# Optimization experiments

Hardware: AMD Instinct MI355X
Metric: run time of the kernel (lower is better)

Reference implementation:

```python
import jax, jax.numpy as jnp
import numpy as np

P = 0.8  # DropConnect keep probability
KERNELS = (3, 2)


def eps_contract(core, x, ks):
    """Contract one EPS core with all sliding ks x ks windows of x.
    core: (out, q**(ks*ks)); x: (b, h, w, q) -> (b, h-ks+1, w-ks+1, out).
    Builds the window tensor-product incrementally (small fixed ks*ks loop)."""
    b, h, w, q = x.shape
    H, W = h - ks + 1, w - ks + 1
    prod = None
    for di in range(ks):
        for dj in range(ks):
            pix = x[:, di:di + H, dj:dj + W, :]  # (b, H, W, q)
            if prod is None:
                prod = pix
            else:
                prod = (prod[..., :, None] * pix[..., None, :]).reshape(b, H, W, -1)
    # prod: (b, H, W, q**(ks*ks))
    return jnp.einsum('bhwk,ok->bhwo', prod, core)


def dropconnect_epses(epses):
    """Bernoulli(P) mask each core's components, rescale by 1/P (training mode)."""
    mkey = jax.random.key(42)
    out = []
    for i, core in enumerate(epses):
        mask = (jax.random.uniform(jax.random.fold_in(mkey, i), core.shape) < P).astype(core.dtype)
        out.append(mask * core / P)
    return out


def setup_inputs() -> dict:
    key = jax.random.key(0)
    k0, k1, k2, k3 = jax.random.split(key, 4)
    b = 128
    x = jax.random.uniform(k0, (b, 28, 28, 2), jnp.float32)  # quantum-encoded image
    d0 = 2 ** (3 * 3)   # 512 : first core input dim (q=2, ks=3)
    d1 = 6 ** (2 * 2)   # 1296: second core input dim (q=6, ks=2)
    eps0 = jax.random.normal(k1, (6, d0), jnp.float32) * d0 ** -0.5
    eps1 = jax.random.normal(k2, (10, d1), jnp.float32) * d1 ** -0.5
    in_features = 25 * 25 * 10  # (28 - (3+2) + 2)^2 * out_q
    W = jax.random.normal(k3, (10, in_features), jnp.float32) * (in_features ** -0.5 / 4.0)
    bias = jnp.zeros((10,), jnp.float32)
    return {"x": x, "eps0": eps0, "eps1": eps1, "W": W, "bias": bias}


def reference(x, eps0, eps1, W, bias):
    e0, e1 = dropconnect_epses((eps0, eps1))
    h = eps_contract(e0, x, KERNELS[0])   # (b, 26, 26, 6)
    h = eps_contract(e1, h, KERNELS[1])   # (b, 25, 25, 10)
    flat = h.reshape(h.shape[0], -1)      # b (h w q)
    return flat @ W.T + bias
```

## Files before the change

### kernel.cpp

```cpp
#include <hip/hip_runtime.h>
#include <hip/hip_bf16.h>
#include <stdint.h>

typedef __attribute__((ext_vector_type(8))) short short8;
typedef __attribute__((ext_vector_type(4))) float floatx4;
typedef __attribute__((ext_vector_type(4))) int intx4;

__device__ float h_g[128 * 4056];
__device__ unsigned short bsw1_g[8192];
__device__ unsigned short bsw2c_g[14400];

__device__ __forceinline__ void threefry2x32(uint32_t k0, uint32_t k1,
                                             uint32_t& x0, uint32_t& x1) {
  const uint32_t ks2 = k0 ^ k1 ^ 0x1BD11BDAu;
  uint32_t ks[3] = {k0, k1, ks2};
  const int rot[8] = {13, 15, 26, 6, 17, 29, 16, 24};
  x0 += ks[0];
  x1 += ks[1];
#pragma unroll
  for (int i = 0; i < 5; ++i) {
#pragma unroll
    for (int j = 0; j < 4; ++j) {
      const int r = rot[(i & 1) * 4 + j];
      x0 += x1;
      x1 = (x1 << r) | (x1 >> (32 - r));
      x1 ^= x0;
    }
    x0 += ks[(i + 1) % 3];
    x1 += ks[(i + 2) % 3] + (uint32_t)(i + 1);
  }
}

struct TFPair { uint32_t x0, x1; };
constexpr TFPair tf_const(uint32_t k0, uint32_t k1, uint32_t x0, uint32_t x1) {
  const uint32_t ks2 = k0 ^ k1 ^ 0x1BD11BDAu;
  uint32_t ks[3] = {k0, k1, ks2};
  const int rot[8] = {13, 15, 26, 6, 17, 29, 16, 24};
  x0 += ks[0];
  x1 += ks[1];
  for (int i = 0; i < 5; ++i) {
    for (int j = 0; j < 4; ++j) {
      const int r = rot[(i & 1) * 4 + j];
      x0 += x1;
      x1 = (x1 << r) | (x1 >> (32 - r));
      x1 ^= x0;
    }
    x0 += ks[(i + 1) % 3];
    x1 += ks[(i + 2) % 3] + (uint32_t)(i + 1);
  }
  return {x0, x1};
}
constexpr TFPair FOLD0 = tf_const(0u, 42u, 0u, 0u);
constexpr TFPair FOLD1 = tf_const(0u, 42u, 0u, 1u);

__device__ __forceinline__ float dropmask(int core, int e, float v) {
  const uint32_t f0 = core ? FOLD1.x0 : FOLD0.x0;
  const uint32_t f1 = core ? FOLD1.x1 : FOLD0.x1;
  uint32_t a = 0u, b = (uint32_t)e;
  threefry2x32(f0, f1, a, b);
  uint32_t bits = a ^ b;
  float u = __uint_as_float((bits >> 9) | 0x3F800000u) - 1.0f;
  float m = (u < 0.8f) ? 1.0f : 0.0f;
  return v * m / 0.8f;
}

__device__ __forceinline__ unsigned short f2bf(float f) {
  uint32_t u = __float_as_uint(f);
  uint32_t r = u + 0x7fffu + ((u >> 16) & 1u);
  return (unsigned short)(r >> 16);
}

union B2I { __hip_bfloat162 b; int i; };
__device__ __forceinline__ int pk_bf16(float lo, float hi) {
  B2I u;
  u.b = __float22bfloat162_rn(make_float2(lo, hi));
  return u.i;
}
union Frag { intx4 i; short8 s; };

__global__ void prep_kernel(const float* __restrict__ eps0,
                            const float* __restrict__ eps1,
                            const float* __restrict__ bias,
                            float* __restrict__ out) {
  int idx = blockIdx.x * 256 + threadIdx.x;
  if (idx < 1280) out[idx] = bias[idx % 10];
  if (idx < 8192) {
    int j = idx & 7, L = (idx >> 3) & 63, c = idx >> 9;
    int o = L & 15, q = L >> 4;
    int k = c * 32 + q * 8 + j;
    float v = 0.0f;
    if (o < 6) {
      int e = o * 512 + k;
      v = dropmask(0, e, eps0[e]);
    }
    bsw1_g[idx] = f2bf(v);
  } else if (idx < 22592) {
    int s = idx - 8192;
    int j = s & 7;
    int wl = (s >> 3) % 40;
    int c = (s >> 3) / 40;
    int o = wl % 10, q = wl / 10;
    int t = 45 * q + c;
    int m = t / 5, nk = 8 * (t % 5) + j;
    float v = 0.0f;
    if (nk < 36) {
      int e = o * 1296 + m * 36 + nk;
      v = dropmask(1, e, eps1[e]);
    }
    bsw2c_g[s] = f2bf(v);
  }
}

__global__ __launch_bounds__(256, 8) void stage1_kernel(
    const float* __restrict__ x) {
  __shared__ intx4 b1s[1024];

  const int b = blockIdx.y;
  const int tid = threadIdx.x;

  {
    const intx4* bsrc1 = (const intx4*)bsw1_g;
#pragma unroll
    for (int i = 0; i < 4; ++i) b1s[i * 256 + tid] = bsrc1[i * 256 + tid];
  }
  __syncthreads();

  const int t1 = blockIdx.x * 4 + (tid >> 6);
  if (t1 >= 43) return;
  const int lane = tid & 63;
  const int col = lane & 15, q = lane >> 4;

  const float2* x2 = (const float2*)x + b * 784;
  const int p_raw = t1 * 16 + col;
  const int p = p_raw < 676 ? p_raw : 675;
  const int ii = p / 26, jj = p - (p / 26) * 26;

  float xv[9][2];
#pragma unroll
  for (int di = 0; di < 3; ++di)
#pragma unroll
    for (int dj = 0; dj < 3; ++dj) {
      float2 v = x2[(ii + di) * 28 + (jj + dj)];
      xv[di * 3 + dj][0] = v.x;
      xv[di * 3 + dj][1] = v.y;
    }

  float w3[8];
#pragma unroll
  for (int j = 0; j < 8; ++j)
    w3[j] = xv[6][(j >> 2) & 1] * xv[7][(j >> 1) & 1] * xv[8][j & 1];

  const float wq = xv[4][(q >> 1) & 1] * xv[5][q & 1];
  float t01[4], t23[4];
#pragma unroll
  for (int a = 0; a < 2; ++a)
#pragma unroll
    for (int d = 0; d < 2; ++d) {
      t01[a * 2 + d] = xv[0][a] * xv[1][d];
      t23[a * 2 + d] = xv[2][a] * xv[3][d] * wq;
    }

  floatx4 acc0 = {0.f, 0.f, 0.f, 0.f};
  floatx4 acc1 = {0.f, 0.f, 0.f, 0.f};
#pragma unroll
  for (int c = 0; c < 16; ++c) {
    Frag bf;
    bf.i = b1s[c * 64 + lane];
    const float w = t01[c >> 2] * t23[c & 3];
    Frag af;
    af.i.x = pk_bf16(w * w3[0], w * w3[1]);
    af.i.y = pk_bf16(w * w3[2], w * w3[3]);
    af.i.z = pk_bf16(w * w3[4], w * w3[5]);
    af.i.w = pk_bf16(w * w3[6], w * w3[7]);
    if (c & 1)
      acc1 = __builtin_amdgcn_mfma_f32_16x16x32_bf16(af.s, bf.s, acc1, 0, 0, 0);
    else
      acc0 = __builtin_amdgcn_mfma_f32_16x16x32_bf16(af.s, bf.s, acc0, 0, 0, 0);
  }
  const floatx4 acc = acc0 + acc1;
  if (col < 6) {
#pragma unroll
    for (int r = 0; r < 4; ++r) {
      const int pp = t1 * 16 + q * 4 + r;
      if (pp < 676) h_g[b * 4056 + pp * 6 + col] = acc[r];
    }
  }
}

__global__ __launch_bounds__(512, 6) void stage2_kernel(
    const float* __restrict__ W, float* __restrict__ out) {
  __shared__ intx4 b2s[1800];
  __shared__ float hs[1092];
  __shared__ float flat_t[8][160];

  const int b = blockIdx.y;
  const int tg = blockIdx.x;
  const int tid = threadIdx.x;
  const int wv = tid >> 6;
  const int lane = tid & 63;
  const int col = lane & 15, q = lane >> 4;
  const int colc = col < 10 ? col : 9;

  {
    const intx4* bsrc2g = (const intx4*)bsw2c_g;
#pragma unroll 1
    for (int i = tid; i < 1800; i += 512) b2s[i] = bsrc2g[i];
  }

  const int r_lo = (tg * 128) / 25;
  const int nrow = (26 - r_lo) < 7 ? (26 - r_lo) : 7;
  const int nflt = nrow * 156;
  for (int i = tid; i < nflt; i += 512) hs[i] = h_g[b * 4056 + r_lo * 156 + i];
  __syncthreads();

  const int tile = tg * 8 + wv;
  const int base2 = tile * 16;
  const int p_raw = base2 + col;
  const int p = p_raw < 625 ? p_raw : 624;
  const int prow = (p * 41) >> 10;
  const int pcol = p - prow * 25;
  const int lr = prow - r_lo;
  const int hbase = (lr * 26 + pcol) * 6;

  float h10r[6], h11r[6];
#pragma unroll
  for (int t = 0; t < 6; ++t) {
    h10r[t] = hs[hbase + 156 + t];
    h11r[t] = hs[hbase + 162 + t];
  }

  floatx4 acc0 = {0.f, 0.f, 0.f, 0.f};
  floatx4 acc1 = {0.f, 0.f, 0.f, 0.f};
#pragma unroll
  for (int d = 0; d < 9; ++d) {
    const int m = 9 * q + d;
    const int ia = (m * 43) >> 8;
    const int ic = m - ia * 6;
    const float p01 = hs[hbase + ia] * hs[hbase + 6 + ic];
    float ph[6];
#pragma unroll
    for (int a = 0; a < 6; ++a) ph[a] = p01 * h10r[a];
#pragma unroll
    for (int e = 0; e < 5; ++e) {
      Frag bf;
      bf.i = b2s[(d * 5 + e) * 40 + q * 10 + colc];
      const int n0 = 8 * e;
      float av[8];
#pragma unroll
      for (int j = 0; j < 8; ++j) {
        const int n = n0 + j;
        av[j] = (n < 36) ? ph[n / 6] * h11r[n % 6] : 0.0f;
      }
      Frag af;
      af.i.x = pk_bf16(av[0], av[1]);
      af.i.y = pk_bf16(av[2], av[3]);
      af.i.z = pk_bf16(av[4], av[5]);
      af.i.w = pk_bf16(av[6], av[7]);
      if (e & 1)
        acc1 = __builtin_amdgcn_mfma_f32_16x16x32_bf16(af.s, bf.s, acc1, 0, 0, 0);
      else
        acc0 = __builtin_amdgcn_mfma_f32_16x16x32_bf16(af.s, bf.s, acc0, 0, 0, 0);
    }
  }
  const floatx4 acc = acc0 + acc1;

  if (col < 10) {
#pragma unroll
    for (int r = 0; r < 4; ++r) {
      const int lp = q * 4 + r;
      flat_t[wv][lp * 10 + col] = (base2 + lp < 625) ? acc[r] : 0.0f;
    }
  }

  float a10[10];
#pragma unroll
  for (int o = 0; o < 10; ++o) a10[o] = 0.0f;
#pragma unroll
  for (int fi = 0; fi < 3; ++fi) {
    const int f = fi * 64 + lane;
    if (f < 160) {
      const float v = flat_t[wv][f];
      int gf = base2 * 10 + f;
      gf = gf < 6250 ? gf : 6249;
#pragma unroll
      for (int o = 0; o < 10; ++o) a10[o] += v * W[o * 6250 + gf];
    }
  }
#pragma unroll
  for (int o = 0; o < 10; ++o) {
#pragma unroll
    for (int s = 32; s > 0; s >>= 1) a10[o] += __shfl_xor(a10[o], s, 64);
  }
  float myv = a10[0];
#pragma unroll
  for (int o = 1; o < 10; ++o) myv = (lane == o) ? a10[o] : myv;
  if (lane < 10) atomicAdd(&out[b * 10 + lane], myv);
}

extern "C" void kernel_launch(void* const* d_in, const int* in_sizes, int n_in,
                              void* d_out, int out_size, void* d_ws,
                              size_t ws_size, hipStream_t stream) {
  const float* x = (const float*)d_in[0];
  const float* eps0 = (const float*)d_in[1];
  const float* eps1 = (const float*)d_in[2];
  const float* W = (const float*)d_in[3];
  const float* bias = (const float*)d_in[4];
  float* out = (float*)d_out;
  (void)d_ws; (void)ws_size;

  hipLaunchKernelGGL(prep_kernel, dim3(89), dim3(256), 0, stream, eps0, eps1,
                     bias, out);
  hipLaunchKernelGGL(stage1_kernel, dim3(11, 128), dim3(256), 0, stream, x);
  hipLaunchKernelGGL(stage2_kernel, dim3(5, 128), dim3(512), 0, stream, W,
                     out);
}
```

Measured before the change: 87.93 us.

## Split final linear layer out of stage2 into a separate reduction kernel

Stage2 now writes its flattened activations to a global buffer instead of doing the dot product with W and atomically adding into the output. A new linear_kernel, one block per batch row, computes the 10 outputs with a block reduction and adds the bias, which removes the atomics and the bias pre-initialisation in prep. The cost is an extra kernel launch and a round trip of about 3.2 MB of activations through global memory.

Measured after the change: 93.90 us. 1.07x slower.

```diff
diff --git a/kernel.cpp b/kernel.cpp
--- a/kernel.cpp
+++ b/kernel.cpp
@@ -7,6 +7,7 @@
 typedef __attribute__((ext_vector_type(4))) int intx4;
 
 __device__ float h_g[128 * 4056];
+__device__ float flat_g[128 * 6400];
 __device__ unsigned short bsw1_g[8192];
 __device__ unsigned short bsw2c_g[14400];
 
@@ -79,11 +80,8 @@
 union Frag { intx4 i; short8 s; };
 
 __global__ void prep_kernel(const float* __restrict__ eps0,
-                            const float* __restrict__ eps1,
-                            const float* __restrict__ bias,
-                            float* __restrict__ out) {
+                            const float* __restrict__ eps1) {
   int idx = blockIdx.x * 256 + threadIdx.x;
-  if (idx < 1280) out[idx] = bias[idx % 10];
   if (idx < 8192) {
     int j = idx & 7, L = (idx >> 3) & 63, c = idx >> 9;
     int o = L & 15, q = L >> 4;
@@ -188,7 +186,7 @@
 }
 
 __global__ __launch_bounds__(512, 6) void stage2_kernel(
-    const float* __restrict__ W, float* __restrict__ out) {
+    float* __restrict__ outdummy) {
   __shared__ intx4 b2s[1800];
   __shared__ float hs[1092];
   __shared__ float flat_t[8][160];
@@ -200,6 +198,7 @@
   const int lane = tid & 63;
   const int col = lane & 15, q = lane >> 4;
   const int colc = col < 10 ? col : 9;
+  (void)outdummy;
 
   {
     const intx4* bsrc2g = (const intx4*)bsw2c_g;
@@ -272,29 +271,48 @@
     }
   }
 
-  float a10[10];
-#pragma unroll
-  for (int o = 0; o < 10; ++o) a10[o] = 0.0f;
-#pragma unroll
-  for (int fi = 0; fi < 3; ++fi) {
-    const int f = fi * 64 + lane;
-    if (f < 160) {
-      const float v = flat_t[wv][f];
-      int gf = base2 * 10 + f;
-      gf = gf < 6250 ? gf : 6249;
-#pragma unroll
-      for (int o = 0; o < 10; ++o) a10[o] += v * W[o * 6250 + gf];
-    }
+  float* dst = flat_g + b * 6400 + base2 * 10;
+#pragma unroll
+  for (int i = 0; i < 3; ++i) {
+    const int f = i * 64 + lane;
+    if (f < 160) dst[f] = flat_t[wv][f];
+  }
+}
+
+__global__ __launch_bounds__(512, 4) void linear_kernel(
+    const float* __restrict__ W, const float* __restrict__ bias,
+    float* __restrict__ out) {
+  __shared__ float red[8][10];
+  const int b = blockIdx.x;
+  const int tid = threadIdx.x;
+  const int lane = tid & 63;
+  const int wv = tid >> 6;
+
+  const float* flat = flat_g + b * 6400;
+  float acc[10];
+#pragma unroll
+  for (int o = 0; o < 10; ++o) acc[o] = 0.0f;
+  for (int f = tid; f < 6250; f += 512) {
+    const float v = flat[f];
+#pragma unroll
+    for (int o = 0; o < 10; ++o) acc[o] += v * W[o * 6250 + f];
   }
 #pragma unroll
   for (int o = 0; o < 10; ++o) {
 #pragma unroll
-    for (int s = 32; s > 0; s >>= 1) a10[o] += __shfl_xor(a10[o], s, 64);
-  }
-  float myv = a10[0];
-#pragma unroll
-  for (int o = 1; o < 10; ++o) myv = (lane == o) ? a10[o] : myv;
-  if (lane < 10) atomicAdd(&out[b * 10 + lane], myv);
+    for (int s = 32; s > 0; s >>= 1) acc[o] += __shfl_xor(acc[o], s, 64);
+  }
+  if (lane == 0) {
+#pragma unroll
+    for (int o = 0; o < 10; ++o) red[wv][o] = acc[o];
+  }
+  __syncthreads();
+  if (tid < 10) {
+    float r = bias[tid];
+#pragma unroll
+    for (int ww = 0; ww < 8; ++ww) r += red[ww][tid];
+    out[b * 10 + tid] = r;
+  }
 }
 
 extern "C" void kernel_launch(void* const* d_in, const int* in_sizes, int n_in,
@@ -308,9 +326,9 @@
   float* out = (float*)d_out;
   (void)d_ws; (void)ws_size;
 
-  hipLaunchKernelGGL(prep_kernel, dim3(89), dim3(256), 0, stream, eps0, eps1,
-                     bias, out);
+  hipLaunchKernelGGL(prep_kernel, dim3(89), dim3(256), 0, stream, eps0, eps1);
   hipLaunchKernelGGL(stage1_kernel, dim3(11, 128), dim3(256), 0, stream, x);
-  hipLaunchKernelGGL(stage2_kernel, dim3(5, 128), dim3(512), 0, stream, W,
+  hipLaunchKernelGGL(stage2_kernel, dim3(5, 128), dim3(512), 0, stream, out);
+  hipLaunchKernelGGL(linear_kernel, dim3(128), dim3(512), 0, stream, W, bias,
                      out);
 }
```

## Fuse stage1 into stage2, computing first-layer rows directly into shared memory

Applied to the files above, without the earlier changes.

Merges the two convolution kernels into one. Each stage2 block now computes the stage1 output rows it needs (with halo) straight into LDS instead of reading them from a global intermediate buffer. This removes one kernel launch and the global write/read of the hidden activations. In exchange, halo rows are recomputed across neighbouring blocks, and the weight fragments are now read from global/L2 rather than staged in LDS, with occupancy lowered to 5 blocks per unit.

After: 92.85 us. 1.06x slower.

```diff
diff --git a/kernel.cpp b/kernel.cpp
--- a/kernel.cpp
+++ b/kernel.cpp
@@ -6,7 +6,6 @@
 typedef __attribute__((ext_vector_type(4))) float floatx4;
 typedef __attribute__((ext_vector_type(4))) int intx4;
 
-__device__ float h_g[128 * 4056];
 __device__ unsigned short bsw1_g[8192];
 __device__ unsigned short bsw2c_g[14400];
 
@@ -111,85 +110,9 @@
   }
 }
 
-__global__ __launch_bounds__(256, 8) void stage1_kernel(
-    const float* __restrict__ x) {
-  __shared__ intx4 b1s[1024];
-
-  const int b = blockIdx.y;
-  const int tid = threadIdx.x;
-
-  {
-    const intx4* bsrc1 = (const intx4*)bsw1_g;
-#pragma unroll
-    for (int i = 0; i < 4; ++i) b1s[i * 256 + tid] = bsrc1[i * 256 + tid];
-  }
-  __syncthreads();
-
-  const int t1 = blockIdx.x * 4 + (tid >> 6);
-  if (t1 >= 43) return;
-  const int lane = tid & 63;
-  const int col = lane & 15, q = lane >> 4;
-
-  const float2* x2 = (const float2*)x + b * 784;
-  const int p_raw = t1 * 16 + col;
-  const int p = p_raw < 676 ? p_raw : 675;
-  const int ii = p / 26, jj = p - (p / 26) * 26;
-
-  float xv[9][2];
-#pragma unroll
-  for (int di = 0; di < 3; ++di)
-#pragma unroll
-    for (int dj = 0; dj < 3; ++dj) {
-      float2 v = x2[(ii + di) * 28 + (jj + dj)];
-      xv[di * 3 + dj][0] = v.x;
-      xv[di * 3 + dj][1] = v.y;
-    }
-
-  float w3[8];
-#pragma unroll
-  for (int j = 0; j < 8; ++j)
-    w3[j] = xv[6][(j >> 2) & 1] * xv[7][(j >> 1) & 1] * xv[8][j & 1];
-
-  const float wq = xv[4][(q >> 1) & 1] * xv[5][q & 1];
-  float t01[4], t23[4];
-#pragma unroll
-  for (int a = 0; a < 2; ++a)
-#pragma unroll
-    for (int d = 0; d < 2; ++d) {
-      t01[a * 2 + d] = xv[0][a] * xv[1][d];
-      t23[a * 2 + d] = xv[2][a] * xv[3][d] * wq;
-    }
-
-  floatx4 acc0 = {0.f, 0.f, 0.f, 0.f};
-  floatx4 acc1 = {0.f, 0.f, 0.f, 0.f};
-#pragma unroll
-  for (int c = 0; c < 16; ++c) {
-    Frag bf;
-    bf.i = b1s[c * 64 + lane];
-    const float w = t01[c >> 2] * t23[c & 3];
-    Frag af;
-    af.i.x = pk_bf16(w * w3[0], w * w3[1]);
-    af.i.y = pk_bf16(w * w3[2], w * w3[3]);
-    af.i.z = pk_bf16(w * w3[4], w * w3[5]);
-    af.i.w = pk_bf16(w * w3[6], w * w3[7]);
-    if (c & 1)
-      acc1 = __builtin_amdgcn_mfma_f32_16x16x32_bf16(af.s, bf.s, acc1, 0, 0, 0);
-    else
-      acc0 = __builtin_amdgcn_mfma_f32_16x16x32_bf16(af.s, bf.s, acc0, 0, 0, 0);
-  }
-  const floatx4 acc = acc0 + acc1;
-  if (col < 6) {
-#pragma unroll
-    for (int r = 0; r < 4; ++r) {
-      const int pp = t1 * 16 + q * 4 + r;
-      if (pp < 676) h_g[b * 4056 + pp * 6 + col] = acc[r];
-    }
-  }
-}
-
-__global__ __launch_bounds__(512, 6) void stage2_kernel(
-    const float* __restrict__ W, float* __restrict__ out) {
-  __shared__ intx4 b2s[1800];
+__global__ __launch_bounds__(512, 5) void merged_kernel(
+    const float* __restrict__ x, const float* __restrict__ W,
+    float* __restrict__ out) {
   __shared__ float hs[1092];
   __shared__ float flat_t[8][160];
 
@@ -199,20 +122,76 @@
   const int wv = tid >> 6;
   const int lane = tid & 63;
   const int col = lane & 15, q = lane >> 4;
-  const int colc = col < 10 ? col : 9;
-
-  {
-    const intx4* bsrc2g = (const intx4*)bsw2c_g;
-#pragma unroll 1
-    for (int i = tid; i < 1800; i += 512) b2s[i] = bsrc2g[i];
-  }
 
   const int r_lo = (tg * 128) / 25;
   const int nrow = (26 - r_lo) < 7 ? (26 - r_lo) : 7;
-  const int nflt = nrow * 156;
-  for (int i = tid; i < nflt; i += 512) hs[i] = h_g[b * 4056 + r_lo * 156 + i];
+  const int pbase = r_lo * 26;
+  const int nspan = nrow * 26;
+  const int ntiles1 = (nspan + 15) >> 4;
+
+  const float2* x2 = (const float2*)x + b * 784;
+  const intx4* bsrc1 = (const intx4*)bsw1_g;
+#pragma unroll 1
+  for (int t1 = wv; t1 < ntiles1; t1 += 8) {
+    const int pl_raw = t1 * 16 + col;
+    const int pl = pl_raw < nspan ? pl_raw : nspan - 1;
+    const int p = pbase + pl;
+    const int ii = p / 26, jj = p - (p / 26) * 26;
+
+    float xv[9][2];
+#pragma unroll
+    for (int di = 0; di < 3; ++di)
+#pragma unroll
+      for (int dj = 0; dj < 3; ++dj) {
+        float2 v = x2[(ii + di) * 28 + (jj + dj)];
+        xv[di * 3 + dj][0] = v.x;
+        xv[di * 3 + dj][1] = v.y;
+      }
+
+    float w3[8];
+#pragma unroll
+    for (int j = 0; j < 8; ++j)
+      w3[j] = xv[6][(j >> 2) & 1] * xv[7][(j >> 1) & 1] * xv[8][j & 1];
+
+    const float wq = xv[4][(q >> 1) & 1] * xv[5][q & 1];
+    float t01[4], t23[4];
+#pragma unroll
+    for (int a = 0; a < 2; ++a)
+#pragma unroll
+      for (int d = 0; d < 2; ++d) {
+        t01[a * 2 + d] = xv[0][a] * xv[1][d];
+        t23[a * 2 + d] = xv[2][a] * xv[3][d] * wq;
+      }
+
+    floatx4 acc0 = {0.f, 0.f, 0.f, 0.f};
+    floatx4 acc1 = {0.f, 0.f, 0.f, 0.f};
+#pragma unroll
+    for (int c = 0; c < 16; ++c) {
+      Frag bf;
+      bf.i = bsrc1[c * 64 + lane];
+      const float w = t01[c >> 2] * t23[c & 3];
+      Frag af;
+      af.i.x = pk_bf16(w * w3[0], w * w3[1]);
+      af.i.y = pk_bf16(w * w3[2], w * w3[3]);
+      af.i.z = pk_bf16(w * w3[4], w * w3[5]);
+      af.i.w = pk_bf16(w * w3[6], w * w3[7]);
+      if (c & 1)
+        acc1 = __builtin_amdgcn_mfma_f32_16x16x32_bf16(af.s, bf.s, acc1, 0, 0, 0);
+      else
+        acc0 = __builtin_amdgcn_mfma_f32_16x16x32_bf16(af.s, bf.s, acc0, 0, 0, 0);
+    }
+    const floatx4 acc = acc0 + acc1;
+    if (col < 6) {
+#pragma unroll
+      for (int r = 0; r < 4; ++r) {
+        const int ppl = t1 * 16 + q * 4 + r;
+        if (ppl < nspan) hs[ppl * 6 + col] = acc[r];
+      }
+    }
+  }
   __syncthreads();
 
+  const int colc = col < 10 ? col : 9;
   const int tile = tg * 8 + wv;
   const int base2 = tile * 16;
   const int p_raw = base2 + col;
@@ -229,6 +208,7 @@
     h11r[t] = hs[hbase + 162 + t];
   }
 
+  const intx4* bsrc2 = (const intx4*)bsw2c_g;
   floatx4 acc0 = {0.f, 0.f, 0.f, 0.f};
   floatx4 acc1 = {0.f, 0.f, 0.f, 0.f};
 #pragma unroll
@@ -243,7 +223,7 @@
 #pragma unroll
     for (int e = 0; e < 5; ++e) {
       Frag bf;
-      bf.i = b2s[(d * 5 + e) * 40 + q * 10 + colc];
+      bf.i = bsrc2[(d * 5 + e) * 40 + q * 10 + colc];
       const int n0 = 8 * e;
       float av[8];
 #pragma unroll
@@ -310,7 +290,6 @@
 
   hipLaunchKernelGGL(prep_kernel, dim3(89), dim3(256), 0, stream, eps0, eps1,
                      bias, out);
-  hipLaunchKernelGGL(stage1_kernel, dim3(11, 128), dim3(256), 0, stream, x);
-  hipLaunchKernelGGL(stage2_kernel, dim3(5, 128), dim3(512), 0, stream, W,
+  hipLaunchKernelGGL(merged_kernel, dim3(5, 128), dim3(512), 0, stream, x, W,
                      out);
 }
```
